# Kernel optimization log

Hardware: AMD Instinct MI355X
Metric: run time of the kernel (lower is better)

Reference implementation:

```python
import jax, jax.numpy as jnp
import numpy as np

N_HEAD = 8


def _axial_attn(x, wq, wk, wv, fw, fb, axis):
    # x: (B, T, H, W, C); axis is the axial axis in (B, nh, T, H, W, d): 2=T, 3=H, 4=W
    B, T, H, W, C = x.shape
    d = C // N_HEAD

    def heads(y):
        # (B,T,H,W,C) -> (B, nh, T, H, W, d)
        return jnp.moveaxis(y.reshape(B, T, H, W, N_HEAD, d), -2, 1)

    q, k, v = heads(x @ wq), heads(x @ wk), heads(x @ wv)
    # restrict attention to the axial axis: move it to -2, all other dims are batch
    q = jnp.moveaxis(q, axis, -2)
    k = jnp.moveaxis(k, axis, -2)
    v = jnp.moveaxis(v, axis, -2)
    scale = 1.0 / jnp.sqrt(jnp.asarray(d, x.dtype))
    scores = jnp.einsum('...ld,...md->...lm', q * scale, k)
    att = jax.nn.softmax(scores, axis=-1)
    o = jnp.einsum('...lm,...md->...ld', att, v)
    o = jnp.moveaxis(o, -2, axis)            # restore axial axis position
    o = jnp.moveaxis(o, 1, -2).reshape(B, T, H, W, C)  # merge heads
    return o @ fw + fb


def setup_inputs() -> dict:
    key = jax.random.key(0)
    ks = jax.random.split(key, 16)
    C = 512
    x = jax.random.normal(ks[0], (4, C, 16, 32, 32), jnp.float32)
    s = 0.02

    def w(k):
        return jax.random.normal(k, (C, C), jnp.float32) * s

    inp = {'x': x}
    i = 1
    for ax in ('w', 'h', 't'):
        inp[f'wq_{ax}'] = w(ks[i])
        inp[f'wk_{ax}'] = w(ks[i + 1])
        inp[f'wv_{ax}'] = w(ks[i + 2])
        inp[f'fc_{ax}'] = w(ks[i + 3])
        inp[f'fb_{ax}'] = jnp.zeros((C,), jnp.float32)
        i += 4
    return inp


def reference(x, wq_w, wk_w, wv_w, fc_w, fb_w,
              wq_h, wk_h, wv_h, fc_h, fb_h,
              wq_t, wk_t, wv_t, fc_t, fb_t):
    xt = jnp.moveaxis(x, 1, -1)  # (B, C, T, H, W) -> (B, T, H, W, C)
    out = (_axial_attn(xt, wq_w, wk_w, wv_w, fc_w, fb_w, 4)   # attend along W
           + _axial_attn(xt, wq_h, wk_h, wv_h, fc_h, fb_h, 3)  # attend along H
           + _axial_attn(xt, wq_t, wk_t, wv_t, fc_t, fb_t, 2))  # attend along T
    return jnp.moveaxis(out, -1, 1)  # back to (B, C, T, H, W)
```

## Files before the change

### kernel.cpp

```cpp
#include <hip/hip_runtime.h>
#include <stdint.h>

typedef __attribute__((ext_vector_type(8))) short bf16x8;
typedef __attribute__((ext_vector_type(4))) float f32x4;

static __device__ __forceinline__ short f2bf(float f) {
  uint32_t u = __builtin_bit_cast(uint32_t, f);
  u += 0x7fffu + ((u >> 16) & 1u);
  return (short)(u >> 16);
}

static __device__ __forceinline__ void gload_lds16(const void* g, void* l) {
  __builtin_amdgcn_global_load_lds((const __attribute__((address_space(1))) void*)g,
                                   (__attribute__((address_space(3))) void*)l, 16, 0, 0);
}

#define GFENCE asm volatile("" ::: "memory")

__global__ __launch_bounds__(256) void transpose_x_k(const float* __restrict__ x,
                                                     short* __restrict__ xb) {
  __shared__ float t[64][65];
  const int pt = blockIdx.x, ct = blockIdx.y, b = blockIdx.z;
  const int tid = threadIdx.x;
#pragma unroll
  for (int i = 0; i < 16; i++) {
    int cc = i * 4 + (tid >> 6);
    int pp = tid & 63;
    t[cc][pp] = x[(size_t)(b * 512 + ct * 64 + cc) * 16384 + pt * 64 + pp];
  }
  __syncthreads();
#pragma unroll
  for (int i = 0; i < 2; i++) {
    int seg = i * 256 + tid;
    int pw = seg >> 3, c8 = seg & 7;
    short tmp[8];
#pragma unroll
    for (int k = 0; k < 8; k++) tmp[k] = f2bf(t[c8 * 8 + k][pw]);
    *(uint4*)&xb[(size_t)(b * 16384 + pt * 64 + pw) * 512 + ct * 64 + c8 * 8] =
        *(const uint4*)tmp;
  }
}

struct WPtrs {
  const float* src[12];
  short* dst[12];
  int ld[12];
};

__global__ __launch_bounds__(256) void transpose_w_k(WPtrs P) {
  __shared__ float t[64][65];
  const int kt = blockIdx.x, nt = blockIdx.y, z = blockIdx.z;
  const float* src = P.src[z];
  short* dst = P.dst[z];
  const int ld = P.ld[z];
  const int tid = threadIdx.x;
#pragma unroll
  for (int i = 0; i < 16; i++) {
    int kk = i * 4 + (tid >> 6);
    int nn = tid & 63;
    t[kk][nn] = src[(kt * 64 + kk) * 512 + nt * 64 + nn];
  }
  __syncthreads();
#pragma unroll
  for (int i = 0; i < 2; i++) {
    int seg = i * 256 + tid;
    int nn = seg >> 3, k8 = seg & 7;
    short tmp[8];
#pragma unroll
    for (int k = 0; k < 8; k++) tmp[k] = f2bf(t[k8 * 8 + k][nn]);
    *(uint4*)&dst[(size_t)(nt * 64 + nn) * ld + kt * 64 + k8 * 8] = *(const uint4*)tmp;
  }
}

__global__ void bsum_k(const float* a, const float* b, const float* c, float* o) {
  int i = blockIdx.x * 256 + threadIdx.x;
  if (i < 512) o[i] = a[i] + b[i] + c[i];
}

#define READ_B(DST, b, kh)                                                     \
  do {                                                                         \
    _Pragma("unroll") for (int ni = 0; ni < 4; ++ni) DST[ni] =                 \
        *(const bf16x8*)(smem + ((b) * 4 + 2 + (kh)) * 16384 + boff +          \
                         ni * 1024);                                           \
  } while (0)

#define READ_A(DST, b, kh, mq)                                                 \
  do {                                                                         \
    _Pragma("unroll") for (int mi = 0; mi < 4; ++mi) DST[mi] =                 \
        *(const bf16x8*)(smem + ((b) * 4 + (kh)) * 16384 + aoff +              \
                         ((mq) * 4 + mi) * 1024);                              \
  } while (0)

#define MFMAX(mq, AF, BF)                                                      \
  do {                                                                         \
    __builtin_amdgcn_s_setprio(1);                                             \
    _Pragma("unroll") for (int mi = 0; mi < 4; ++mi)                           \
        _Pragma("unroll") for (int ni = 0; ni < 4; ++ni) acc[(mq) * 4 + mi]    \
            [ni] = __builtin_amdgcn_mfma_f32_16x16x32_bf16(                    \
                AF[mi], BF[ni], acc[(mq) * 4 + mi][ni], 0, 0, 0);              \
    __builtin_amdgcn_s_setprio(0);                                             \
    GFENCE;                                                                    \
  } while (0)

#define TILE_RA(b, b2, W1, W3, S0, S1, S2, S3, RA)                             \
  do {                                                                         \
                            \
    __builtin_amdgcn_s_barrier();                                              \
    GFENCE;                                                                    \
    READ_A(afB, b, 0, 1);                                                      \
    S0;                                                                        \
    GFENCE;                                                                    \
    MFMAX(0, afA, bfA);                                                        \
                     \
    asm volatile("s_waitcnt vmcnt(" W1 ")" ::: "memory");                      \
    __builtin_amdgcn_s_barrier();                                              \
    GFENCE;                                                                    \
    READ_B(bfB, b, 1);                                                         \
    READ_A(afA, b, 1, 0);                                                      \
    S1;                                                                        \
    GFENCE;                                                                    \
    MFMAX(1, afB, bfA);                                                        \
                            \
    __builtin_amdgcn_s_barrier();                                              \
    GFENCE;                                                                    \
    READ_A(afB, b, 1, 1);                                                      \
    S2;                                                                        \
    GFENCE;                                                                    \
    MFMAX(0, afA, bfB);                                                        \
                 \
    asm volatile("s_waitcnt vmcnt(" W3 ")" ::: "memory");                      \
    __builtin_amdgcn_s_barrier();                                              \
    GFENCE;                                                                    \
    RA;                                                                        \
    S3;                                                                        \
    GFENCE;                                                                    \
    MFMAX(1, afB, bfB);                                                        \
  } while (0)

template <int MODE>
__global__ __launch_bounds__(512, 2) void gemm256_k(const short* __restrict__ A,
                                                    int lda,
                                                    const short* __restrict__ B,
                                                    int ldb, void* __restrict__ Dp,
                                                    int K, int ldd,
                                                    const float* __restrict__ bsum,
                                                    int GN) {
  extern __shared__ char smem[];
  const int tid = threadIdx.x;
  const int lane = tid & 63, wave = tid >> 6;
  const int wr = wave >> 2, wc = wave & 3;
  const int r4 = lane & 15, kl = lane >> 4;

  int bid = blockIdx.x;
  const int cpx = gridDim.x >> 3;
  bid = (bid & 7) * cpx + (bid >> 3);
  int bm, bn;
  if constexpr (MODE == 0) {
    bn = bid % GN;
    bm = bid / GN;
  } else {
    bm = bid & 1;
    bn = bid >> 1;
  }

  const int NT = K >> 6;

  const int srow = tid >> 2;
  const int schk = (tid & 3) ^ ((tid >> 3) & 3);
  const short* gA0 = A + (size_t)(bm * 256 + srow) * lda + schk * 8;
  const short* gB0 = B + (size_t)(bn * 256 + srow) * ldb + schk * 8;

  auto stage = [&](int tt, int x) {
    const short* g = (x < 2) ? gA0 : gB0;
    const size_t rstep = (size_t)128 * ((x < 2) ? lda : ldb);
    const size_t koff = (size_t)tt * 64 + (x & 1) * 32;
    char* ldst = smem + (((tt & 1) * 4 + x) * 16384) + wave * 1024;
#pragma unroll
    for (int i = 0; i < 2; ++i)
      gload_lds16(g + i * rstep + koff, ldst + i * 8192);
  };

  const int kls = kl ^ ((r4 >> 1) & 3);
  const int aoff = wr * 8192 + r4 * 64 + kls * 16;
  const int boff = wc * 4096 + r4 * 64 + kls * 16;

  f32x4 acc[8][4];
#pragma unroll
  for (int i = 0; i < 8; ++i)
#pragma unroll
    for (int j = 0; j < 4; ++j) acc[i][j] = (f32x4){0.f, 0.f, 0.f, 0.f};
  bf16x8 afA[4], afB[4], bfA[4], bfB[4];

  stage(0, 0);
  stage(0, 2);
  stage(0, 1);
  stage(0, 3);
  stage(1, 0);
  stage(1, 2);
  asm volatile("s_waitcnt vmcnt(8)" ::: "memory");
  __builtin_amdgcn_s_barrier();
  GFENCE;
  READ_B(bfA, 0, 0);
  READ_A(afA, 0, 0, 0);
  GFENCE;

  int t = 0;
  for (; t < NT - 2; ++t) {
    const int b = t & 1, b2 = b ^ 1;
    TILE_RA(b, b2, "6", "6", stage(t + 1, 1), stage(t + 1, 3), stage(t + 2, 0),
            stage(t + 2, 2), {
              READ_B(bfA, b2, 0);
              READ_A(afA, b2, 0, 0);
            });
  }
  {
    const int b = t & 1, b2 = b ^ 1;
    TILE_RA(b, b2, "6", "4", stage(t + 1, 1), stage(t + 1, 3), (void)0, (void)0, {
      READ_B(bfA, b2, 0);
      READ_A(afA, b2, 0, 0);
    });
    ++t;
  }
  {
    const int b = t & 1, b2 = b ^ 1;
    TILE_RA(b, b2, "0", "0", (void)0, (void)0, (void)0, (void)0, (void)0);
  }

  const int m0 = wr * 128 + kl * 4;
  const int n0 = wc * 64 + r4;
  if (MODE == 0) {
    short* D = (short*)Dp;
#pragma unroll
    for (int mi = 0; mi < 8; ++mi)
#pragma unroll
      for (int ni = 0; ni < 4; ++ni)
#pragma unroll
        for (int r = 0; r < 4; ++r) {
          int row = bm * 256 + m0 + mi * 16 + r;
          int col = bn * 256 + n0 + ni * 16;
          D[(size_t)row * ldd + col] = f2bf(acc[mi][ni][r]);
        }
  } else {
    float* D = (float*)Dp + (size_t)((bn * 256) >> 14) * 8388608;
#pragma unroll
    for (int mi = 0; mi < 8; ++mi)
#pragma unroll
      for (int ni = 0; ni < 4; ++ni)
#pragma unroll
        for (int r = 0; r < 4; ++r) {
          int c = bm * 256 + m0 + mi * 16 + r;
          int n = (bn * 256 + n0 + ni * 16) & 16383;
          D[(size_t)c * 16384 + n] = acc[mi][ni][r] + bsum[c];
        }
  }
}

template <int L>
__global__ __launch_bounds__(256) void attn_mfma_k(const short* __restrict__ qkv,
                                                   short* __restrict__ o, int Adiv,
                                                   int Bmul, int Cmul, int stride,
                                                   int obase) {
  constexpr int MT = L / 16;
  constexpr int PITCH = 40;
  __shared__ short lds[4 * (32 + 64) * PITCH];
  const int tid = threadIdx.x;
  const int lane = tid & 63, wave = tid >> 6;
  short* p_lds = lds + wave * (96 * PITCH);
  short* vt = p_lds + 32 * PITCH;

  const int wid = blockIdx.x * 4 + wave;
  const int s = wid >> 3, head = wid & 7;
  const int base = (s / Adiv) * Bmul + (s % Adiv) * Cmul;
  const int r4 = lane & 15, kl = lane >> 4;

  if constexpr (L == 16) {
    for (int i = lane; i < 96 * PITCH; i += 64) p_lds[i] = 0;
  }

  bf16x8 qf[MT][2], kf[MT][2];
#pragma unroll
  for (int mi = 0; mi < MT; ++mi)
#pragma unroll
    for (int ks = 0; ks < 2; ++ks) {
      size_t nrow = (size_t)(base + (mi * 16 + r4) * stride) * 1536 + head * 64 +
                    ks * 32 + kl * 8;
      qf[mi][ks] = *(const bf16x8*)&qkv[nrow];
      kf[mi][ks] = *(const bf16x8*)&qkv[nrow + 512];
    }

#pragma unroll
  for (int it = 0; it < L / 8; ++it) {
    int j = (lane >> 3) + it * 8;
    uint4 u = *(const uint4*)&qkv[(size_t)(base + j * stride) * 1536 + 1024 +
                                  head * 64 + (lane & 7) * 8];
    ushort e[8];
    *(uint4*)e = u;
#pragma unroll
    for (int q = 0; q < 8; ++q) vt[((lane & 7) * 8 + q) * PITCH + j] = (short)e[q];
  }

  f32x4 sacc[MT][MT];
#pragma unroll
  for (int i = 0; i < MT; ++i)
#pragma unroll
    for (int j = 0; j < MT; ++j) sacc[i][j] = (f32x4){0.f, 0.f, 0.f, 0.f};
#pragma unroll
  for (int mi = 0; mi < MT; ++mi)
#pragma unroll
    for (int ni = 0; ni < MT; ++ni)
#pragma unroll
      for (int ks = 0; ks < 2; ++ks)
        sacc[mi][ni] = __builtin_amdgcn_mfma_f32_16x16x32_bf16(
            qf[mi][ks], kf[ni][ks], sacc[mi][ni], 0, 0, 0);

#pragma unroll
  for (int mi = 0; mi < MT; ++mi) {
    float mx[4], sm[4];
#pragma unroll
    for (int r = 0; r < 4; ++r) {
      float m = sacc[mi][0][r];
      if (MT == 2) m = fmaxf(m, sacc[mi][1][r]);
#pragma unroll
      for (int d = 1; d < 16; d <<= 1) m = fmaxf(m, __shfl_xor(m, d));
      mx[r] = m;
    }
#pragma unroll
    for (int ni = 0; ni < MT; ++ni)
#pragma unroll
      for (int r = 0; r < 4; ++r)
        sacc[mi][ni][r] = __expf((sacc[mi][ni][r] - mx[r]) * 0.125f);
#pragma unroll
    for (int r = 0; r < 4; ++r) {
      float t = sacc[mi][0][r];
      if (MT == 2) t += sacc[mi][1][r];
#pragma unroll
      for (int d = 1; d < 16; d <<= 1) t += __shfl_xor(t, d);
      sm[r] = 1.0f / t;
    }
#pragma unroll
    for (int ni = 0; ni < MT; ++ni)
#pragma unroll
      for (int r = 0; r < 4; ++r)
        p_lds[(mi * 16 + kl * 4 + r) * PITCH + ni * 16 + r4] =
            f2bf(sacc[mi][ni][r] * sm[r]);
  }
  asm volatile("s_waitcnt lgkmcnt(0)" ::: "memory");

  bf16x8 paf[MT], vbf[4];
#pragma unroll
  for (int mi = 0; mi < MT; ++mi)
    paf[mi] = *(const bf16x8*)&p_lds[(mi * 16 + r4) * PITCH + kl * 8];
#pragma unroll
  for (int nd = 0; nd < 4; ++nd)
    vbf[nd] = *(const bf16x8*)&vt[(nd * 16 + r4) * PITCH + kl * 8];
  f32x4 oacc[MT][4];
#pragma unroll
  for (int i = 0; i < MT; ++i)
#pragma unroll
    for (int j = 0; j < 4; ++j) oacc[i][j] = (f32x4){0.f, 0.f, 0.f, 0.f};
#pragma unroll
  for (int mi = 0; mi < MT; ++mi)
#pragma unroll
    for (int nd = 0; nd < 4; ++nd)
      oacc[mi][nd] = __builtin_amdgcn_mfma_f32_16x16x32_bf16(paf[mi], vbf[nd],
                                                             oacc[mi][nd], 0, 0, 0);

#pragma unroll
  for (int mi = 0; mi < MT; ++mi)
#pragma unroll
    for (int r = 0; r < 4; ++r) {
      int n = base + (mi * 16 + kl * 4 + r) * stride;
      size_t ob = (size_t)n * 1536 + obase + head * 64 + r4;
#pragma unroll
      for (int nd = 0; nd < 4; ++nd) o[ob + nd * 16] = f2bf(oacc[mi][nd][r]);
    }
}

extern "C" void kernel_launch(void* const* d_in, const int* in_sizes, int n_in,
                              void* d_out, int out_size, void* d_ws, size_t ws_size,
                              hipStream_t stream) {
  const float* x = (const float*)d_in[0];
  const float* wq[3];
  const float* wk[3];
  const float* wv[3];
  const float* fc[3];
  const float* fb[3];
  for (int a = 0; a < 3; a++) {
    wq[a] = (const float*)d_in[1 + a * 5];
    wk[a] = (const float*)d_in[2 + a * 5];
    wv[a] = (const float*)d_in[3 + a * 5];
    fc[a] = (const float*)d_in[4 + a * 5];
    fb[a] = (const float*)d_in[5 + a * 5];
  }
  char* ws = (char*)d_ws;
  short* xb = (short*)(ws);
  short* qkv = (short*)(ws + 67108864);
  short* wqkvt = (short*)(ws + 268435456);
  short* fctA = (short*)(ws + 273154048);
  float* bsum = (float*)(ws + 274726912);
  short* ob = (short*)(ws + 274728960);
  float* out = (float*)d_out;

  (void)hipFuncSetAttribute((const void*)&gemm256_k<0>,
                            hipFuncAttributeMaxDynamicSharedMemorySize, 131072);
  (void)hipFuncSetAttribute((const void*)&gemm256_k<1>,
                            hipFuncAttributeMaxDynamicSharedMemorySize, 131072);

  WPtrs P;
  for (int a = 0; a < 3; a++) {
    P.src[a * 4 + 0] = wq[a];
    P.src[a * 4 + 1] = wk[a];
    P.src[a * 4 + 2] = wv[a];
    P.src[a * 4 + 3] = fc[a];
    P.dst[a * 4 + 0] = wqkvt + (size_t)a * 1536 * 512;
    P.dst[a * 4 + 1] = wqkvt + (size_t)a * 1536 * 512 + 512 * 512;
    P.dst[a * 4 + 2] = wqkvt + (size_t)a * 1536 * 512 + 2 * 512 * 512;
    P.dst[a * 4 + 3] = fctA + a * 512;
    P.ld[a * 4 + 0] = 512;
    P.ld[a * 4 + 1] = 512;
    P.ld[a * 4 + 2] = 512;
    P.ld[a * 4 + 3] = 1536;
  }
  transpose_w_k<<<dim3(8, 8, 12), 256, 0, stream>>>(P);
  bsum_k<<<dim3(2), 256, 0, stream>>>(fb[0], fb[1], fb[2], bsum);
  transpose_x_k<<<dim3(256, 8, 4), 256, 0, stream>>>(x, xb);

  const int Ad[3] = {1, 32, 1024};
  const int Bm_[3] = {32, 1024, 16384};
  const int Cm[3] = {0, 1, 1};
  const int St[3] = {1, 32, 1024};
  const int Ls[3] = {32, 32, 16};

  for (int a = 0; a < 3; a++) {
    gemm256_k<0><<<dim3(1536), 512, 131072, stream>>>(
        xb, 512, wqkvt + (size_t)a * 1536 * 512, 512, (void*)qkv, 512, 1536,
        nullptr, 6);
    if (Ls[a] == 32)
      attn_mfma_k<32><<<dim3(4096), 256, 0, stream>>>(qkv, ob, Ad[a], Bm_[a], Cm[a],
                                                      St[a], a * 512);
    else
      attn_mfma_k<16><<<dim3(8192), 256, 0, stream>>>(qkv, ob, Ad[a], Bm_[a], Cm[a],
                                                      St[a], a * 512);
  }
  gemm256_k<1><<<dim3(512), 512, 131072, stream>>>(
      fctA, 1536, ob, 1536, (void*)out, 1536, 0, bsum, 0);
}
```

Baseline: 690.5 us.

## Use separate QKV buffers per axis and write attention output in place

When the workspace is large enough, the change gives each axis its own QKV buffer. All three QKV GEMMs run first, then the three attention kernels, and each attention kernel writes its output in place into its own QKV buffer. The final projection GEMM takes three B pointers and picks the source per K-tile, so no separate concatenated output buffer is needed. This is meant to improve back-to-back kernel scheduling and cut the footprint of the output buffer, but it needs a bigger workspace and depends on in-place attention writes being safe.

```diff
diff --git a/kernel.cpp b/kernel.cpp
--- a/kernel.cpp
+++ b/kernel.cpp
@@ -141,6 +141,8 @@
 __global__ __launch_bounds__(512, 2) void gemm256_k(const short* __restrict__ A,
                                                     int lda,
                                                     const short* __restrict__ B,
+                                                    const short* __restrict__ B1,
+                                                    const short* __restrict__ B2,
                                                     int ldb, void* __restrict__ Dp,
                                                     int K, int ldd,
                                                     const float* __restrict__ bsum,
@@ -169,11 +171,30 @@
   const int schk = (tid & 3) ^ ((tid >> 3) & 3);
   const short* gA0 = A + (size_t)(bm * 256 + srow) * lda + schk * 8;
   const short* gB0 = B + (size_t)(bn * 256 + srow) * ldb + schk * 8;
+  const short* gB1p = nullptr;
+  const short* gB2p = nullptr;
+  if constexpr (MODE == 1) {
+    gB1p = B1 + (size_t)(bn * 256 + srow) * ldb + schk * 8;
+    gB2p = B2 + (size_t)(bn * 256 + srow) * ldb + schk * 8;
+  }
 
   auto stage = [&](int tt, int x) {
-    const short* g = (x < 2) ? gA0 : gB0;
+    const short* g;
+    size_t koff;
     const size_t rstep = (size_t)128 * ((x < 2) ? lda : ldb);
-    const size_t koff = (size_t)tt * 64 + (x & 1) * 32;
+    if (x < 2) {
+      g = gA0;
+      koff = (size_t)tt * 64 + (x & 1) * 32;
+    } else {
+      if (MODE == 0) {
+        g = gB0;
+        koff = (size_t)tt * 64 + (x & 1) * 32;
+      } else {
+        const int sel = tt >> 3;
+        g = (sel == 0) ? gB0 : (sel == 1) ? gB1p : gB2p;
+        koff = (size_t)(tt & 7) * 64 + (x & 1) * 32;
+      }
+    }
     char* ldst = smem + (((tt & 1) * 4 + x) * 16384) + wave * 1024;
 #pragma unroll
     for (int i = 0; i < 2; ++i)
@@ -394,12 +415,16 @@
   }
   char* ws = (char*)d_ws;
   short* xb = (short*)(ws);
-  short* qkv = (short*)(ws + 67108864);
-  short* wqkvt = (short*)(ws + 268435456);
-  short* fctA = (short*)(ws + 273154048);
-  float* bsum = (float*)(ws + 274726912);
-  short* ob = (short*)(ws + 274728960);
+  short* wqkvt = (short*)(ws + 67108864);
+  short* fctA = (short*)(ws + 71827456);
+  float* bsum = (float*)(ws + 73400320);
+  short* q0 = (short*)(ws + 73402368);
+  short* obuf = (short*)(ws + 274728960);
+  short* q2 = (short*)(ws + 476055552);
   float* out = (float*)d_out;
+
+  const bool f3 = ws_size >= 677382144ull;
+  short* q1 = f3 ? obuf : q0;
 
   (void)hipFuncSetAttribute((const void*)&gemm256_k<0>,
                             hipFuncAttributeMaxDynamicSharedMemorySize, 131072);
@@ -431,17 +456,36 @@
   const int St[3] = {1, 32, 1024};
   const int Ls[3] = {32, 32, 16};
 
-  for (int a = 0; a < 3; a++) {
-    gemm256_k<0><<<dim3(1536), 512, 131072, stream>>>(
-        xb, 512, wqkvt + (size_t)a * 1536 * 512, 512, (void*)qkv, 512, 1536,
-        nullptr, 6);
-    if (Ls[a] == 32)
-      attn_mfma_k<32><<<dim3(4096), 256, 0, stream>>>(qkv, ob, Ad[a], Bm_[a], Cm[a],
-                                                      St[a], a * 512);
-    else
-      attn_mfma_k<16><<<dim3(8192), 256, 0, stream>>>(qkv, ob, Ad[a], Bm_[a], Cm[a],
-                                                      St[a], a * 512);
-  }
-  gemm256_k<1><<<dim3(512), 512, 131072, stream>>>(
-      fctA, 1536, ob, 1536, (void*)out, 1536, 0, bsum, 0);
-}
+  if (f3) {
+    short* qs[3] = {q0, q1, q2};
+    for (int a = 0; a < 3; a++)
+      gemm256_k<0><<<dim3(1536), 512, 131072, stream>>>(
+          xb, 512, wqkvt + (size_t)a * 1536 * 512, nullptr, nullptr, 512,
+          (void*)qs[a], 512, 1536, nullptr, 6);
+    for (int a = 0; a < 3; a++) {
+      if (Ls[a] == 32)
+        attn_mfma_k<32><<<dim3(4096), 256, 0, stream>>>(qs[a], qs[a], Ad[a], Bm_[a],
+                                                        Cm[a], St[a], 0);
+      else
+        attn_mfma_k<16><<<dim3(8192), 256, 0, stream>>>(qs[a], qs[a], Ad[a], Bm_[a],
+                                                        Cm[a], St[a], 0);
+    }
+    gemm256_k<1><<<dim3(512), 512, 131072, stream>>>(
+        fctA, 1536, q0, q1, q2, 1536, (void*)out, 1536, 0, bsum, 0);
+  } else {
+    short* ob = obuf;
+    for (int a = 0; a < 3; a++) {
+      gemm256_k<0><<<dim3(1536), 512, 131072, stream>>>(
+          xb, 512, wqkvt + (size_t)a * 1536 * 512, nullptr, nullptr, 512,
+          (void*)q0, 512, 1536, nullptr, 6);
+      if (Ls[a] == 32)
+        attn_mfma_k<32><<<dim3(4096), 256, 0, stream>>>(q0, ob, Ad[a], Bm_[a],
+                                                        Cm[a], St[a], a * 512);
+      else
+        attn_mfma_k<16><<<dim3(8192), 256, 0, stream>>>(q0, ob, Ad[a], Bm_[a],
+                                                        Cm[a], St[a], a * 512);
+    }
+    gemm256_k<1><<<dim3(512), 512, 131072, stream>>>(
+        fctA, 1536, ob, ob + 512, ob + 1024, 1536, (void*)out, 1536, 0, bsum, 0);
+  }
+}
```

Result: slower. 742.0 us (+7.5%).
